# Kernel optimization log

Measured on AMD Instinct MI355X. Metric: run time of the kernel, lower is better.

The kernel has to match this reference:

```python
import jax, jax.numpy as jnp
import numpy as np

B, N, NPOINT, NSAMPLE = 4, 8192, 2048, 32
RADIUS = 0.5
IN_DIM, OUT_DIM, EXP = 64, 128, 4
GROUPS, EPS = 8, 1e-5


def fps(xyz, npoint):
    # xyz: [B,3,N] -> idx [B,npoint]. Deterministic start at index 0
    # (torch version uses a random start; math otherwise identical).
    b, _, n = xyz.shape
    binds = jnp.arange(b)

    def step(carry, _):
        dist_min, far = carry
        centroid = xyz[binds, :, far]                      # [B,3]
        d = jnp.sum((xyz - centroid[:, :, None]) ** 2, 1)  # [B,N]
        dist_min = jnp.minimum(dist_min, d)
        new_far = jnp.argmax(dist_min, axis=-1).astype(jnp.int32)
        return (dist_min, new_far), far

    init = (jnp.full((b, n), 1e10, dtype=xyz.dtype), jnp.zeros((b,), jnp.int32))
    _, idx = jax.lax.scan(step, init, None, length=npoint)
    return idx.T  # [B, npoint]


def gather(points, idx):
    # points: [B,C,N], idx: [B, ...] -> [B, C, ...]
    return jax.vmap(lambda p, i: p[:, i])(points, idx)


def ball_query(radius, nsample, xyz, new_xyz):
    # xyz: [B,3,N], new_xyz: [B,3,S] -> group_idx [B,S,nsample]
    n = xyz.shape[2]
    sq_s = jnp.sum(new_xyz ** 2, axis=1)  # [B,S]
    sq_n = jnp.sum(xyz ** 2, axis=1)      # [B,N]
    d = sq_s[:, :, None] + sq_n[:, None, :] - 2.0 * jnp.einsum('bcs,bcn->bsn', new_xyz, xyz)
    ar = jnp.arange(n, dtype=jnp.int32)
    idxv = jnp.where(d <= radius * radius, ar[None, None, :], n)  # out-of-ball -> N
    neg, _ = jax.lax.top_k(-idxv, nsample)  # nsample smallest indices
    gi = -neg                               # ascending, matches sort()[..., :nsample]
    first = gi[:, :, :1]
    first = jnp.where(first == n, 0, first)
    gi = jnp.where(gi == n, first, gi)
    return gi


def group_norm(x, gamma, beta):
    # x: [B,C,*spatial]; normalize per (group, all spatial)
    b, c = x.shape[0], x.shape[1]
    sp = x.shape[2:]
    xg = x.reshape(b, GROUPS, -1)
    mu = xg.mean(-1, keepdims=True)
    var = xg.var(-1, keepdims=True)
    xg = (xg - mu) * jax.lax.rsqrt(var + EPS)
    x = xg.reshape(b, c, *sp)
    gshape = (1, c) + (1,) * len(sp)
    return x * gamma.reshape(gshape) + beta.reshape(gshape)


def setup_inputs() -> dict:
    key = jax.random.key(0)
    ks = jax.random.split(key, 10)
    sc = lambda k, shape, s: jax.random.normal(k, shape, jnp.float32) * s
    ed = OUT_DIM * EXP
    return {
        'xyz': jax.random.normal(ks[0], (B, 3, N), jnp.float32),
        'points': jax.random.normal(ks[1], (B, IN_DIM, N), jnp.float32),
        't_emb': jax.random.normal(ks[2], (B, OUT_DIM), jnp.float32),
        'c_emb': jax.random.normal(ks[3], (B, OUT_DIM), jnp.float32),
        'w_mlp': sc(ks[4], (OUT_DIM, IN_DIM + 3), 0.1), 'b_mlp': jnp.zeros((OUT_DIM,), jnp.float32),
        'g0': jnp.ones((OUT_DIM,), jnp.float32), 'be0': jnp.zeros((OUT_DIM,), jnp.float32),
        'w1': sc(ks[5], (ed, OUT_DIM), 0.1), 'b1': jnp.zeros((ed,), jnp.float32),
        'g1': jnp.ones((ed,), jnp.float32), 'be1': jnp.zeros((ed,), jnp.float32),
        'w2': sc(ks[6], (OUT_DIM, ed), 0.1), 'b2': jnp.zeros((OUT_DIM,), jnp.float32),
        'g2': jnp.ones((OUT_DIM,), jnp.float32), 'be2': jnp.zeros((OUT_DIM,), jnp.float32),
        'wt': sc(ks[7], (2 * OUT_DIM, OUT_DIM), 0.02), 'bt': jnp.zeros((2 * OUT_DIM,), jnp.float32),
        'wc': sc(ks[8], (2 * OUT_DIM, OUT_DIM), 0.02), 'bc': jnp.zeros((2 * OUT_DIM,), jnp.float32),
    }


def reference(xyz, points, t_emb, c_emb, w_mlp, b_mlp, g0, be0, w1, b1, g1, be1, w2, b2, g2, be2, wt, bt, wc, bc):
    idx = fps(xyz, NPOINT)              # [B,S]
    new_xyz = gather(xyz, idx)          # [B,3,S]
    gi = ball_query(RADIUS, NSAMPLE, xyz, new_xyz)   # [B,S,ns]
    grouped_xyz = gather(xyz, gi)                    # [B,3,S,ns]
    gxn = grouped_xyz - new_xyz[:, :, :, None]
    gp = gather(points, gi)                          # [B,C,S,ns]
    feat = jnp.concatenate([gxn, gp], axis=1)        # [B,C+3,S,ns]
    x = jnp.einsum('oc,bcsk->bosk', w_mlp, feat) + b_mlp[None, :, None, None]
    x = jax.nn.silu(group_norm(x, g0, be0))
    x = x.max(axis=3)                                # [B,O,S]
    # InvResMLP with dual FiLM
    identity = x
    h = jnp.einsum('oc,bcs->bos', w1, x) + b1[None, :, None]
    h = jax.nn.silu(group_norm(h, g1, be1))
    h = jnp.einsum('oc,bcs->bos', w2, h) + b2[None, :, None]
    h = group_norm(h, g2, be2)
    st, sht = jnp.split(t_emb @ wt.T + bt, 2, axis=1)
    sc_, shc = jnp.split(c_emb @ wc.T + bc, 2, axis=1)
    scale = (st + sc_)[:, :, None]
    shift = (sht + shc)[:, :, None]
    new_points = h * (1.0 + scale) + shift + identity
    return (new_xyz, new_points)
```

## Files before the change

### kernel.cpp

```cpp
#include <hip/hip_runtime.h>
#include <math.h>

#define BB 4
#define NN 8192
#define SS 2048
#define KK 32
#define NGR 8

__global__ void k_sqn(const float* __restrict__ xyz, float* __restrict__ sqn) {
  int i = blockIdx.x * 256 + threadIdx.x;
  if (i >= BB * NN) return;
  int b = i >> 13, n = i & (NN - 1);
  const float* p = xyz + (size_t)b * 3 * NN;
  float x = p[n], y = p[NN + n], z = p[2 * NN + n];
  sqn[i] = __fadd_rn(__fadd_rn(__fmul_rn(x, x), __fmul_rn(y, y)), __fmul_rn(z, z));
}

__global__ void k_tr(const float* __restrict__ pts, float* __restrict__ ptst) {
  __shared__ float tile[64][65];
  int b = blockIdx.y;
  int n0 = blockIdx.x * 64;
  int t = threadIdx.x;
  {
    int n = t & 63, cq = t >> 6;
    for (int j = 0; j < 16; ++j) {
      int c = cq * 16 + j;
      tile[c][n] = pts[((size_t)b * 64 + c) * NN + n0 + n];
    }
  }
  __syncthreads();
  {
    int c = t & 63, nq = t >> 6;
    for (int j = 0; j < 16; ++j) {
      int nn2 = nq * 16 + j;
      ptst[((size_t)b * NN + n0 + nn2) * 64 + c] = tile[c][nn2];
    }
  }
}

__global__ void k_wt(const float* __restrict__ src, float* __restrict__ dst, int rows, int cols) {
  int i = blockIdx.x * 256 + threadIdx.x;
  if (i >= rows * cols) return;
  int r = i / cols, c = i - r * cols;
  dst[c * rows + r] = src[i];
}

__global__ void k_mod(const float* __restrict__ te, const float* __restrict__ ce,
                      const float* __restrict__ wt, const float* __restrict__ bt,
                      const float* __restrict__ wc, const float* __restrict__ bc,
                      float* __restrict__ scl, float* __restrict__ shf) {
  int t = blockIdx.x * 256 + threadIdx.x;
  if (t >= BB * 128) return;
  int b = t >> 7, o = t & 127;
  const float* tb = te + b * 128;
  const float* cb = ce + b * 128;
  float s1 = 0.f, s2 = 0.f, h1 = 0.f, h2 = 0.f;
  for (int c = 0; c < 128; ++c) {
    float tv = tb[c], cv = cb[c];
    s1 = fmaf(tv, wt[o * 128 + c], s1);
    h1 = fmaf(tv, wt[(o + 128) * 128 + c], h1);
    s2 = fmaf(cv, wc[o * 128 + c], s2);
    h2 = fmaf(cv, wc[(o + 128) * 128 + c], h2);
  }
  scl[t] = s1 + bt[o] + s2 + bc[o];
  shf[t] = h1 + bt[o + 128] + h2 + bc[o + 128];
}

template <int CTRL>
__device__ __forceinline__ unsigned long long kmax_dpp(unsigned long long key) {
  int lo = (int)(unsigned)(key & 0xffffffffull);
  int hi = (int)(unsigned)(key >> 32);
  int olo = __builtin_amdgcn_update_dpp(lo, lo, CTRL, 0xf, 0xf, false);
  int ohi = __builtin_amdgcn_update_dpp(hi, hi, CTRL, 0xf, 0xf, false);
  unsigned long long other =
      ((unsigned long long)(unsigned)ohi << 32) | (unsigned)olo;
  return other > key ? other : key;
}

#define FT 256
#define FPT (NN / FT)

__global__ __launch_bounds__(FT, 1) void k_fps(const float* __restrict__ xyz,
                                               float* __restrict__ newxyz) {
  int b = blockIdx.x;
  int t = threadIdx.x;
  const float* gx = xyz + (size_t)b * 3 * NN;
  const float* gy = gx + NN;
  const float* gz = gx + 2 * NN;
  float px[FPT], py[FPT], pz[FPT], dm[FPT];
#pragma unroll
  for (int j = 0; j < FPT; ++j) {
    int p = t + j * FT;
    px[j] = gx[p]; py[j] = gy[p]; pz[j] = gz[p];
    dm[j] = 1e10f;
  }
  __shared__ unsigned long long wk[2][4];
  int far = 0;
  float* ox = newxyz + (size_t)b * 3 * SS;
  for (int k = 0; k < SS; ++k) {
    float cx = gx[far], cy = gy[far], cz = gz[far];
    if (t == 0) { ox[k] = cx; ox[SS + k] = cy; ox[2 * SS + k] = cz; }
    float bv = -1.f;
    int bp = 0;
#pragma unroll
    for (int j = 0; j < FPT; ++j) {
      float dx = __fsub_rn(px[j], cx);
      float dy = __fsub_rn(py[j], cy);
      float dz = __fsub_rn(pz[j], cz);
      float d = __fadd_rn(__fadd_rn(__fmul_rn(dx, dx), __fmul_rn(dy, dy)), __fmul_rn(dz, dz));
      float m = fminf(dm[j], d);
      dm[j] = m;
      if (m > bv) { bv = m; bp = t + j * FT; }
    }
    unsigned long long key =
        ((unsigned long long)__float_as_uint(bv) << 32) | (unsigned)(NN - 1 - bp);
    key = kmax_dpp<0xB1>(key);
    key = kmax_dpp<0x4E>(key);
    key = kmax_dpp<0x141>(key);
    key = kmax_dpp<0x140>(key);
    key = kmax_dpp<0x142>(key);
    key = kmax_dpp<0x143>(key);
    if ((t & 63) == 63) wk[k & 1][t >> 6] = key;
    __syncthreads();
    unsigned long long k0 = wk[k & 1][0], k1 = wk[k & 1][1];
    unsigned long long k2 = wk[k & 1][2], k3 = wk[k & 1][3];
    unsigned long long ka = k0 > k1 ? k0 : k1;
    unsigned long long kb = k2 > k3 ? k2 : k3;
    unsigned long long kg = ka > kb ? ka : kb;
    far = NN - 1 - (int)(unsigned)(kg & 0xffffffffull);
    far = __builtin_amdgcn_readfirstlane(far);
  }
}

__global__ __launch_bounds__(256) void k_ballq(const float* __restrict__ xyz,
                                               const float* __restrict__ sqn,
                                               const float* __restrict__ newxyz,
                                               int* __restrict__ gi) {
  int wid = (blockIdx.x * 256 + threadIdx.x) >> 6;
  int lane = threadIdx.x & 63;
  if (wid >= BB * SS) return;
  int b = wid >> 11, s = wid & (SS - 1);
  const float* nx = newxyz + (size_t)b * 3 * SS;
  float sx = nx[s], sy = nx[SS + s], sz = nx[2 * SS + s];
  float ss = __fadd_rn(__fadd_rn(__fmul_rn(sx, sx), __fmul_rn(sy, sy)), __fmul_rn(sz, sz));
  const float* gx = xyz + (size_t)b * 3 * NN;
  const float* gy = gx + NN;
  const float* gz = gx + 2 * NN;
  const float* sn = sqn + (size_t)b * NN;
  int* go = gi + (size_t)wid * KK;
  int found = 0, first = 0;
  for (int n0 = 0; n0 < NN && found < KK; n0 += 64) {
    int n = n0 + lane;
    float x = gx[n], y = gy[n], z = gz[n];
    float ip = __fmul_rn(sx, x);
    ip = __fmaf_rn(sy, y, ip);
    ip = __fmaf_rn(sz, z, ip);
    float d = __fsub_rn(__fadd_rn(ss, sn[n]), __fmul_rn(2.0f, ip));
    bool pred = (d <= 0.25f);
    unsigned long long m = __ballot(pred);
    if (found == 0 && m) first = n0 + __ffsll((unsigned long long)m) - 1;
    if (pred) {
      int pos = found + __popcll(m & ((1ull << lane) - 1ull));
      if (pos < KK) go[pos] = n;
    }
    found += __popcll(m);
  }
  for (int p = found + lane; p < KK; p += 64) go[p] = first;
}

template <int PASS>
__global__ __launch_bounds__(256) void k_mlp0(
    const float* __restrict__ xyz, const float* __restrict__ ptst,
    const float* __restrict__ newxyz, const int* __restrict__ gi,
    const float* __restrict__ w0, const float* __restrict__ b0,
    double* __restrict__ dst, const float* __restrict__ fmu, const float* __restrict__ frs,
    const float* __restrict__ g0, const float* __restrict__ be0,
    float* __restrict__ xp) {
  __shared__ __align__(16) float w0L[128 * 67];
  __shared__ __align__(16) float featL[67 * 36];
  __shared__ int giL[KK];
  __shared__ float sS[NGR], sQ[NGR];
  __shared__ float maxL[128];
  int t = threadIdx.x;
  int bs = blockIdx.x;
  int b = bs >> 11;
  int s = bs & (SS - 1);
  for (int i = t; i < 128 * 67; i += 256) w0L[i] = w0[i];
  if (t < KK) giL[t] = gi[(size_t)bs * KK + t];
  if (PASS == 0 && t < NGR) { sS[t] = 0.f; sQ[t] = 0.f; }
  __syncthreads();
  {
    int k = t & 31, q = t >> 5;
    int idx = giL[k];
    const float4* src = (const float4*)(ptst + ((size_t)b * NN + idx) * 64 + q * 8);
    float4 v0 = src[0], v1 = src[1];
    int cb = 3 + q * 8;
    featL[(cb + 0) * 36 + k] = v0.x;
    featL[(cb + 1) * 36 + k] = v0.y;
    featL[(cb + 2) * 36 + k] = v0.z;
    featL[(cb + 3) * 36 + k] = v0.w;
    featL[(cb + 4) * 36 + k] = v1.x;
    featL[(cb + 5) * 36 + k] = v1.y;
    featL[(cb + 6) * 36 + k] = v1.z;
    featL[(cb + 7) * 36 + k] = v1.w;
    if (q == 0) {
      const float* gx = xyz + (size_t)b * 3 * NN;
      const float* nx = newxyz + (size_t)b * 3 * SS;
      featL[0 * 36 + k] = gx[idx] - nx[s];
      featL[1 * 36 + k] = gx[NN + idx] - nx[SS + s];
      featL[2 * 36 + k] = gx[2 * NN + idx] - nx[2 * SS + s];
    }
  }
  __syncthreads();
  int o = t & 127, kh = t >> 7;
  float acc[16];
#pragma unroll
  for (int j = 0; j < 16; ++j) acc[j] = 0.f;
  const float* wrow = w0L + o * 67;
  const float* fb = featL + kh * 16;
  for (int c = 0; c < 67; ++c) {
    float w = wrow[c];
    const float4* f4 = (const float4*)(fb + c * 36);
    float4 a = f4[0], b4 = f4[1], c4 = f4[2], d4 = f4[3];
    acc[0] = fmaf(w, a.x, acc[0]);    acc[1] = fmaf(w, a.y, acc[1]);
    acc[2] = fmaf(w, a.z, acc[2]);    acc[3] = fmaf(w, a.w, acc[3]);
    acc[4] = fmaf(w, b4.x, acc[4]);   acc[5] = fmaf(w, b4.y, acc[5]);
    acc[6] = fmaf(w, b4.z, acc[6]);   acc[7] = fmaf(w, b4.w, acc[7]);
    acc[8] = fmaf(w, c4.x, acc[8]);   acc[9] = fmaf(w, c4.y, acc[9]);
    acc[10] = fmaf(w, c4.z, acc[10]); acc[11] = fmaf(w, c4.w, acc[11]);
    acc[12] = fmaf(w, d4.x, acc[12]); acc[13] = fmaf(w, d4.y, acc[13]);
    acc[14] = fmaf(w, d4.z, acc[14]); acc[15] = fmaf(w, d4.w, acc[15]);
  }
  float bb = b0[o];
  int g = o >> 4;
  if (PASS == 0) {
    float ps = 0.f, pq = 0.f;
#pragma unroll
    for (int j = 0; j < 16; ++j) { float v = acc[j] + bb; ps += v; pq += v * v; }
    atomicAdd(&sS[g], ps);
    atomicAdd(&sQ[g], pq);
    __syncthreads();
    if (t < NGR) {
      atomicAdd(&dst[b * NGR + t], (double)sS[t]);
      atomicAdd(&dst[32 + b * NGR + t], (double)sQ[t]);
    }
  } else {
    float mu = fmu[b * NGR + g], rs = frs[b * NGR + g];
    float ga = g0[o], be = be0[o];
    float m = -3.4e38f;
#pragma unroll
    for (int j = 0; j < 16; ++j) {
      float v = acc[j] + bb;
      v = (v - mu) * rs * ga + be;
      v = v / (1.f + expf(-v));
      m = fmaxf(m, v);
    }
    if (kh == 0) maxL[o] = m;
    __syncthreads();
    if (kh == 1) xp[(size_t)bs * 128 + o] = fmaxf(maxL[o], m);
  }
}

__global__ void k_fin(const double* __restrict__ dst, float* __restrict__ fmu,
                      float* __restrict__ frs, double cntInv) {
  int i = threadIdx.x;
  if (i >= BB * NGR) return;
  double m = dst[i] * cntInv;
  double q = dst[32 + i] * cntInv;
  double var = q - m * m;
  fmu[i] = (float)m;
  frs[i] = (float)rsqrt(var + 1e-5);
}

__global__ __launch_bounds__(256) void k_mlp1(
    const float* __restrict__ xp, const float* __restrict__ w1t,
    const float* __restrict__ b1, float* __restrict__ h1, double* __restrict__ dst) {
  __shared__ __align__(16) float xpL[8 * 128];
  __shared__ float sS[NGR], sQ[NGR];
  int t = threadIdx.x;
  int bs0 = blockIdx.x * 8;
  int b = bs0 >> 11;
  if (t < NGR) { sS[t] = 0.f; sQ[t] = 0.f; }
  {
    int idx4 = t >> 5, l = t & 31;
    ((float4*)xpL)[idx4 * 32 + l] = ((const float4*)(xp + (size_t)bs0 * 128))[idx4 * 32 + l];
  }
  __syncthreads();
  float acc0[8], acc1[8];
#pragma unroll
  for (int i = 0; i < 8; ++i) { acc0[i] = 0.f; acc1[i] = 0.f; }
  for (int c4 = 0; c4 < 32; ++c4) {
    float wa0 = w1t[(c4 * 4 + 0) * 512 + t];
    float wa1 = w1t[(c4 * 4 + 1) * 512 + t];
    float wa2 = w1t[(c4 * 4 + 2) * 512 + t];
    float wa3 = w1t[(c4 * 4 + 3) * 512 + t];
    float wb0 = w1t[(c4 * 4 + 0) * 512 + 256 + t];
    float wb1 = w1t[(c4 * 4 + 1) * 512 + 256 + t];
    float wb2 = w1t[(c4 * 4 + 2) * 512 + 256 + t];
    float wb3 = w1t[(c4 * 4 + 3) * 512 + 256 + t];
#pragma unroll
    for (int si = 0; si < 8; ++si) {
      float4 xv = *(const float4*)(xpL + si * 128 + c4 * 4);
      acc0[si] = fmaf(wa0, xv.x, acc0[si]);
      acc0[si] = fmaf(wa1, xv.y, acc0[si]);
      acc0[si] = fmaf(wa2, xv.z, acc0[si]);
      acc0[si] = fmaf(wa3, xv.w, acc0[si]);
      acc1[si] = fmaf(wb0, xv.x, acc1[si]);
      acc1[si] = fmaf(wb1, xv.y, acc1[si]);
      acc1[si] = fmaf(wb2, xv.z, acc1[si]);
      acc1[si] = fmaf(wb3, xv.w, acc1[si]);
    }
  }
  float ba = b1[t], bbv = b1[256 + t];
  float ps0 = 0.f, pq0 = 0.f, ps1 = 0.f, pq1 = 0.f;
#pragma unroll
  for (int si = 0; si < 8; ++si) {
    float va = acc0[si] + ba;
    float vb = acc1[si] + bbv;
    h1[(size_t)(bs0 + si) * 512 + t] = va;
    h1[(size_t)(bs0 + si) * 512 + 256 + t] = vb;
    ps0 += va; pq0 += va * va;
    ps1 += vb; pq1 += vb * vb;
  }
  atomicAdd(&sS[t >> 6], ps0);
  atomicAdd(&sQ[t >> 6], pq0);
  atomicAdd(&sS[4 + (t >> 6)], ps1);
  atomicAdd(&sQ[4 + (t >> 6)], pq1);
  __syncthreads();
  if (t < NGR) {
    atomicAdd(&dst[b * NGR + t], (double)sS[t]);
    atomicAdd(&dst[32 + b * NGR + t], (double)sQ[t]);
  }
}

__global__ __launch_bounds__(256) void k_mlp2(
    const float* __restrict__ h1, const float* __restrict__ w2t,
    const float* __restrict__ b2, const float* __restrict__ fmu1, const float* __restrict__ frs1,
    const float* __restrict__ g1, const float* __restrict__ be1,
    float* __restrict__ h2, double* __restrict__ dst) {
  __shared__ __align__(16) float hL[8 * 512];
  __shared__ float sS[NGR], sQ[NGR];
  int t = threadIdx.x;
  int bs0 = blockIdx.x * 8;
  int b = bs0 >> 11;
  if (t < NGR) { sS[t] = 0.f; sQ[t] = 0.f; }
  {
    int si = t >> 5, l = t & 31;
    int c0 = l * 16;
    int g = c0 >> 6;
    float mu = fmu1[b * NGR + g], rs = frs1[b * NGR + g];
    const float* src = h1 + (size_t)(bs0 + si) * 512 + c0;
#pragma unroll
    for (int j = 0; j < 16; ++j) {
      float v = src[j];
      v = (v - mu) * rs * g1[c0 + j] + be1[c0 + j];
      v = v / (1.f + expf(-v));
      hL[si * 512 + c0 + j] = v;
    }
  }
  __syncthreads();
  int o = t & 127, sh = t >> 7;
  float acc[4] = {0.f, 0.f, 0.f, 0.f};
  for (int c4 = 0; c4 < 128; ++c4) {
    float w0v = w2t[(c4 * 4 + 0) * 128 + o];
    float w1v = w2t[(c4 * 4 + 1) * 128 + o];
    float w2v = w2t[(c4 * 4 + 2) * 128 + o];
    float w3v = w2t[(c4 * 4 + 3) * 128 + o];
#pragma unroll
    for (int m = 0; m < 4; ++m) {
      float4 hq = *(const float4*)(hL + (sh * 4 + m) * 512 + c4 * 4);
      acc[m] = fmaf(w0v, hq.x, acc[m]);
      acc[m] = fmaf(w1v, hq.y, acc[m]);
      acc[m] = fmaf(w2v, hq.z, acc[m]);
      acc[m] = fmaf(w3v, hq.w, acc[m]);
    }
  }
  float bb = b2[o];
  float ps = 0.f, pq = 0.f;
#pragma unroll
  for (int m = 0; m < 4; ++m) {
    float v = acc[m] + bb;
    h2[(size_t)(bs0 + sh * 4 + m) * 128 + o] = v;
    ps += v; pq += v * v;
  }
  atomicAdd(&sS[o >> 4], ps);
  atomicAdd(&sQ[o >> 4], pq);
  __syncthreads();
  if (t < NGR) {
    atomicAdd(&dst[b * NGR + t], (double)sS[t]);
    atomicAdd(&dst[32 + b * NGR + t], (double)sQ[t]);
  }
}

__global__ void k_final(const float* __restrict__ h2, const float* __restrict__ xp,
                        const float* __restrict__ fmu2, const float* __restrict__ frs2,
                        const float* __restrict__ g2, const float* __restrict__ be2,
                        const float* __restrict__ scl, const float* __restrict__ shf,
                        float* __restrict__ out) {
  int f = blockIdx.x * 256 + threadIdx.x;
  if (f >= BB * 128 * SS) return;
  int s = f & (SS - 1);
  int o = (f >> 11) & 127;
  int b = f >> 18;
  int g = o >> 4;
  float v = h2[((size_t)b * SS + s) * 128 + o];
  v = (v - fmu2[b * NGR + g]) * frs2[b * NGR + g] * g2[o] + be2[o];
  float idv = xp[((size_t)b * SS + s) * 128 + o];
  out[f] = v * (1.f + scl[b * 128 + o]) + shf[b * 128 + o] + idv;
}

extern "C" void kernel_launch(void* const* d_in, const int* in_sizes, int n_in,
                              void* d_out, int out_size, void* d_ws, size_t ws_size,
                              hipStream_t stream) {
  const float* xyz = (const float*)d_in[0];
  const float* pts = (const float*)d_in[1];
  const float* te = (const float*)d_in[2];
  const float* ce = (const float*)d_in[3];
  const float* w0 = (const float*)d_in[4];
  const float* b0 = (const float*)d_in[5];
  const float* g0 = (const float*)d_in[6];
  const float* be0 = (const float*)d_in[7];
  const float* w1 = (const float*)d_in[8];
  const float* b1 = (const float*)d_in[9];
  const float* g1 = (const float*)d_in[10];
  const float* be1 = (const float*)d_in[11];
  const float* w2 = (const float*)d_in[12];
  const float* b2 = (const float*)d_in[13];
  const float* g2 = (const float*)d_in[14];
  const float* be2 = (const float*)d_in[15];
  const float* wt = (const float*)d_in[16];
  const float* bt = (const float*)d_in[17];
  const float* wc = (const float*)d_in[18];
  const float* bc = (const float*)d_in[19];

  char* ws = (char*)d_ws;
  size_t off = 0;
  auto alloc = [&](size_t bytes) {
    void* p = ws + off;
    off += (bytes + 255) & ~(size_t)255;
    return p;
  };
  float* ptst = (float*)alloc((size_t)BB * NN * 64 * 4);
  float* sqn = (float*)alloc((size_t)BB * NN * 4);
  int* gi = (int*)alloc((size_t)BB * SS * KK * 4);
  float* xp = (float*)alloc((size_t)BB * SS * 128 * 4);
  float* h1 = (float*)alloc((size_t)BB * SS * 512 * 4);
  float* h2 = (float*)alloc((size_t)BB * SS * 128 * 4);
  float* w1t = (float*)alloc(512 * 128 * 4);
  float* w2t = (float*)alloc(512 * 128 * 4);
  float* scl = (float*)alloc(BB * 128 * 4);
  float* shf = (float*)alloc(BB * 128 * 4);
  double* dstat = (double*)alloc(3 * 64 * 8);
  float* fmu = (float*)alloc(3 * 32 * 4);
  float* frs = (float*)alloc(3 * 32 * 4);

  float* newxyz = (float*)d_out;
  float* outnp = (float*)d_out + (size_t)BB * 3 * SS;

  hipMemsetAsync(dstat, 0, 3 * 64 * 8, stream);
  k_sqn<<<BB * NN / 256, 256, 0, stream>>>(xyz, sqn);
  k_tr<<<dim3(NN / 64, BB), 256, 0, stream>>>(pts, ptst);
  k_wt<<<(512 * 128 + 255) / 256, 256, 0, stream>>>(w1, w1t, 512, 128);
  k_wt<<<(512 * 128 + 255) / 256, 256, 0, stream>>>(w2, w2t, 128, 512);
  k_mod<<<2, 256, 0, stream>>>(te, ce, wt, bt, wc, bc, scl, shf);
  k_fps<<<BB, FT, 0, stream>>>(xyz, newxyz);
  k_ballq<<<BB * SS / 4, 256, 0, stream>>>(xyz, sqn, newxyz, gi);
  k_mlp0<0><<<BB * SS, 256, 0, stream>>>(xyz, ptst, newxyz, gi, w0, b0, dstat, fmu, frs, g0, be0, xp);
  k_fin<<<1, 64, 0, stream>>>(dstat, fmu, frs, 1.0 / (16.0 * SS * KK));
  k_mlp0<1><<<BB * SS, 256, 0, stream>>>(xyz, ptst, newxyz, gi, w0, b0, dstat, fmu, frs, g0, be0, xp);
  k_mlp1<<<BB * SS / 8, 256, 0, stream>>>(xp, w1t, b1, h1, dstat + 64);
  k_fin<<<1, 64, 0, stream>>>(dstat + 64, fmu + 32, frs + 32, 1.0 / (64.0 * SS));
  k_mlp2<<<BB * SS / 8, 256, 0, stream>>>(h1, w2t, b2, fmu + 32, frs + 32, g1, be1, h2, dstat + 128);
  k_fin<<<1, 64, 0, stream>>>(dstat + 128, fmu + 64, frs + 64, 1.0 / (16.0 * SS));
  k_final<<<BB * 128 * SS / 256, 256, 0, stream>>>(h2, xp, fmu + 64, frs + 64, g2, be2, scl, shf, outnp);
}
```

Baseline: 2.697 ms.

## Stage FPS points in shared memory as float4 and double threads per block

The FPS kernel now copies each batch's xyz into a 128KB shared float4 array and runs 512 threads per block instead of 256, keeping only the running min distances in registers. Each iteration reads point coordinates from LDS and fetches the centroid from LDS instead of global memory, and the cross-wave reduction loops over 8 wave keys. The aim is to halve the serial per-thread work per iteration and remove the global load latency for the centroid. The cost is LDS bandwidth for every point read, more waves meeting at the barrier each iteration, and a 128KB shared allocation per block.

```diff
diff --git a/kernel.cpp b/kernel.cpp
--- a/kernel.cpp
+++ b/kernel.cpp
@@ -77,8 +77,9 @@
   return other > key ? other : key;
 }
 
-#define FT 256
+#define FT 512
 #define FPT (NN / FT)
+#define FW (FT / 64)
 
 __global__ __launch_bounds__(FT, 1) void k_fps(const float* __restrict__ xyz,
                                                float* __restrict__ newxyz) {
@@ -87,26 +88,27 @@
   const float* gx = xyz + (size_t)b * 3 * NN;
   const float* gy = gx + NN;
   const float* gz = gx + 2 * NN;
-  float px[FPT], py[FPT], pz[FPT], dm[FPT];
-#pragma unroll
-  for (int j = 0; j < FPT; ++j) {
-    int p = t + j * FT;
-    px[j] = gx[p]; py[j] = gy[p]; pz[j] = gz[p];
-    dm[j] = 1e10f;
-  }
-  __shared__ unsigned long long wk[2][4];
+  __shared__ float4 p4[NN];
+  __shared__ unsigned long long wk[2][FW];
+  for (int i = t; i < NN; i += FT)
+    p4[i] = make_float4(gx[i], gy[i], gz[i], 0.f);
+  float dm[FPT];
+#pragma unroll
+  for (int j = 0; j < FPT; ++j) dm[j] = 1e10f;
+  __syncthreads();
   int far = 0;
   float* ox = newxyz + (size_t)b * 3 * SS;
   for (int k = 0; k < SS; ++k) {
-    float cx = gx[far], cy = gy[far], cz = gz[far];
-    if (t == 0) { ox[k] = cx; ox[SS + k] = cy; ox[2 * SS + k] = cz; }
+    float4 c = p4[far];
+    if (t == 0) { ox[k] = c.x; ox[SS + k] = c.y; ox[2 * SS + k] = c.z; }
     float bv = -1.f;
     int bp = 0;
 #pragma unroll
     for (int j = 0; j < FPT; ++j) {
-      float dx = __fsub_rn(px[j], cx);
-      float dy = __fsub_rn(py[j], cy);
-      float dz = __fsub_rn(pz[j], cz);
+      float4 p = p4[t + j * FT];
+      float dx = __fsub_rn(p.x, c.x);
+      float dy = __fsub_rn(p.y, c.y);
+      float dz = __fsub_rn(p.z, c.z);
       float d = __fadd_rn(__fadd_rn(__fmul_rn(dx, dx), __fmul_rn(dy, dy)), __fmul_rn(dz, dz));
       float m = fminf(dm[j], d);
       dm[j] = m;
@@ -122,11 +124,12 @@
     key = kmax_dpp<0x143>(key);
     if ((t & 63) == 63) wk[k & 1][t >> 6] = key;
     __syncthreads();
-    unsigned long long k0 = wk[k & 1][0], k1 = wk[k & 1][1];
-    unsigned long long k2 = wk[k & 1][2], k3 = wk[k & 1][3];
-    unsigned long long ka = k0 > k1 ? k0 : k1;
-    unsigned long long kb = k2 > k3 ? k2 : k3;
-    unsigned long long kg = ka > kb ? ka : kb;
+    unsigned long long kg = wk[k & 1][0];
+#pragma unroll
+    for (int w = 1; w < FW; ++w) {
+      unsigned long long kw = wk[k & 1][w];
+      kg = kw > kg ? kw : kg;
+    }
     far = NN - 1 - (int)(unsigned)(kg & 0xffffffffull);
     far = __builtin_amdgcn_readfirstlane(far);
   }
```

Measured after the change: 2.673 ms. No clear change (-0.9%).
